# Kernel tuning notes

Measured on AMD Instinct MI355X. Metric: run time of the kernel, lower is better.

Reference implementation:

```python
import jax, jax.numpy as jnp
import numpy as np

NUM_HEADS = 8
MASK_NEG = -1e30


def setup_inputs() -> dict:
    key = jax.random.key(0)
    k1, k2, k3 = jax.random.split(key, 3)
    B, S, D = 8, 2048, 128
    queries = jax.random.normal(k1, (B, S, D), dtype=jnp.float32)
    mask = jnp.ones((B, S), dtype=jnp.float32)
    # kernel_size=1 Conv1D with no bias == dense matmul over last dim
    W_q = jax.random.normal(k2, (D, D), dtype=jnp.float32) * (D ** -0.5)
    W_mem = jax.random.normal(k3, (D, 2 * D), dtype=jnp.float32) * (D ** -0.5)
    return {"queries": queries, "mask": mask, "W_q": W_q, "W_mem": W_mem}


def _split_heads(x, h):
    # [B, S, D] -> [B, h, S, D/h]
    B, S, D = x.shape
    return x.reshape(B, S, h, D // h).transpose(0, 2, 1, 3)


def reference(queries, mask, W_q, W_mem):
    B, S, D = queries.shape
    h = NUM_HEADS
    scale = (D // h) ** -0.5
    memory = jnp.einsum('bsd,de->bse', queries, W_mem)   # [B,S,2D]
    query = jnp.einsum('bsd,de->bse', queries, W_q)      # [B,S,D]
    K, V = jnp.split(memory, 2, axis=2)
    Q = _split_heads(query, h) * scale                   # [B,h,S,dh]
    K = _split_heads(K, h)
    V = _split_heads(V, h)
    logits = jnp.einsum('bhqd,bhkd->bhqk', Q, K)         # [B,h,S,S]
    m = mask.reshape(B, 1, 1, S)
    logits = logits + (1.0 - m) * MASK_NEG
    weights = jax.nn.softmax(logits, axis=-1)
    # dropout is identity at inference (training=None)
    x = jnp.einsum('bhqk,bhkd->bhqd', weights, V)        # [B,h,S,dh]
    return x.transpose(0, 2, 1, 3).reshape(B, S, D)
```

## Files before the change

kernel.cpp:

```cpp
#include <hip/hip_runtime.h>
#include <hip/hip_bf16.h>
#include <stdint.h>

#define B_    8
#define S_    2048
#define D_    128
#define H_    8
#define DH_   16
#define BH_   64
#define E_    384
#define NT_   (S_ / 32)

typedef __attribute__((ext_vector_type(4)))  short short4v;
typedef __attribute__((ext_vector_type(8)))  short short8;
typedef __attribute__((ext_vector_type(4)))  float f32x4;
typedef __attribute__((ext_vector_type(16))) float f32x16;

__device__ inline unsigned short f2b(float f) {
    union { __bf16 h; unsigned short u; } t;
    t.h = (__bf16)f;
    return t.u;
}
__device__ inline float b2f(unsigned short u) {
    union { unsigned u; float f; } x; x.u = ((unsigned)u) << 16; return x.f;
}
__device__ inline int dperm(int d) {
    return (d & 3) | ((d & 8) >> 1) | ((d & 4) << 1);
}

#define EXPB 16250.7346f

__global__ void wtrans_kernel(const float* __restrict__ Wq,
                              const float* __restrict__ Wmem,
                              unsigned short* __restrict__ wt) {
    int e = blockIdx.x, k = threadIdx.x;
    float v = (e < 128) ? Wq[k * 128 + e] : Wmem[k * 256 + (e - 128)];
    wt[e * 128 + k] = f2b(v);
}

__global__ __launch_bounds__(512) void proj_kernel(
        const float* __restrict__ X, const float* __restrict__ mask,
        const unsigned short* __restrict__ wt,
        unsigned short* __restrict__ Qb, unsigned short* __restrict__ Kb,
        unsigned short* __restrict__ Vf) {
    __shared__ unsigned short Xs[64][136];
    __shared__ unsigned short Vs[64][136];
    __shared__ float Ms[64];
    const int tid = threadIdx.x;
    const int b = blockIdx.x & 7, st = blockIdx.x >> 3;
    const int s0 = st * 64;
    const float* Xp = X + ((size_t)b * S_ + s0) * D_;

    for (int i = tid; i < 64 * D_ / 4; i += 512) {
        float4 v = ((const float4*)Xp)[i];
        int row = i >> 5, c4 = (i & 31) * 4;
        Xs[row][c4 + 0] = f2b(v.x); Xs[row][c4 + 1] = f2b(v.y);
        Xs[row][c4 + 2] = f2b(v.z); Xs[row][c4 + 3] = f2b(v.w);
    }
    if (tid < 64) Ms[tid] = mask[(size_t)b * S_ + s0 + tid];
    __syncthreads();

    const int wid = tid >> 6, lane = tid & 63;
    const int lr = lane & 15, lg = lane >> 4;
    const float qscale = 0.25f * 1.44269504088896f;

    for (int ci = 0; ci < 3; ++ci) {
        const int ct = wid + ci * 8;
        const int e0 = ct * 16;
        short4v bfr[8];
        #pragma unroll
        for (int kk = 0; kk < 8; ++kk)
            bfr[kk] = *(const short4v*)&wt[(e0 + lr) * 128 + kk * 16 + lg * 4];
        for (int rt = 0; rt < 4; ++rt) {
            f32x4 acc; acc[0] = acc[1] = acc[2] = acc[3] = 0.f;
            #pragma unroll
            for (int kk = 0; kk < 8; ++kk) {
                short4v a = *(const short4v*)&Xs[rt * 16 + lr][kk * 16 + lg * 4];
                acc = __builtin_amdgcn_mfma_f32_16x16x16bf16_1k(a, bfr[kk], acc, 0, 0, 0);
            }
            const int e = e0 + lr;
            #pragma unroll
            for (int r = 0; r < 4; ++r) {
                const int sl = rt * 16 + lg * 4 + r;
                const float v = acc[r];
                if (e < 128) {
                    int hh = e >> 4, d = dperm(e & 15);
                    Qb[(((size_t)b * H_ + hh) * S_ + s0 + sl) * DH_ + d] = f2b(v * qscale);
                } else if (e < 256) {
                    int ek = e - 128, hh = ek >> 4, d = dperm(ek & 15);
                    Kb[(((size_t)b * H_ + hh) * S_ + s0 + sl) * DH_ + d] = f2b(v);
                } else {
                    Vs[sl][e - 256] = f2b(v);
                }
            }
        }
    }
    __syncthreads();

    for (int j = tid; j < H_ * 2 * 2 * 64; j += 512) {
        const int l = j & 63, f = (j >> 6) & 1, t = (j >> 7) & 1, hh = j >> 8;
        const int q = l & 31, h = l >> 5;
        const int vrow = (q < 16) ? q : 16;
        const int T = st * 2 + t;
        unsigned short* dst =
            Vf + ((((size_t)(b * H_ + hh) * NT_ + T) * 2 + f) * 64 + l) * 8;
        union { unsigned short us[8]; short8 v; } o;
        #pragma unroll
        for (int e = 0; e < 8; ++e) {
            const int p = f * 16 + 8 * h + e;
            const int sl = (p & 16) | dperm(p & 15);
            const int srow = t * 32 + sl;
            const float mk = Ms[srow];
            o.us[e] = f2b((vrow == 16) ? mk : b2f(Vs[srow][hh * 16 + vrow]) * mk);
        }
        *(short8*)dst = o.v;
    }
}

__global__ __launch_bounds__(512, 8) void attn_kernel(
        const unsigned short* __restrict__ Qb, const unsigned short* __restrict__ Kb,
        const unsigned short* __restrict__ Vf, float* __restrict__ out) {
    const int tid = threadIdx.x;
    const int wid = tid >> 6, lane = tid & 63;
    const int q = lane & 31, h = lane >> 5;
    const int p = blockIdx.x;
    const int bh = (p & 7) * 8 + ((p >> 3) & 7);
    const int qt = p >> 6;
    const int q0 = qt * 128 + (wid >> 1) * 32;
    const int ttBase = (wid & 1) * (NT_ / 2);
    const int ttEnd  = ttBase + NT_ / 2;

    const unsigned short* Kp = Kb + (size_t)bh * S_ * DH_ + 8 * h;
    const unsigned short* vfl = Vf + (size_t)bh * NT_ * 1024 + (size_t)lane * 8;

    const short8 qf = *(const short8*)&Qb[((size_t)bh * S_ + q0 + q) * DH_ + 8 * h];

    f32x16 acc, z;
    #pragma unroll
    for (int i = 0; i < 16; ++i) { acc[i] = 0.f; z[i] = 0.f; }

    #pragma unroll 2
    for (int tt = ttBase; tt < ttEnd; ++tt) {
        const short8 kf  = *(const short8*)&Kp[(size_t)(tt * 32 + q) * DH_];
        const short8 va0 = *(const short8*)&vfl[(size_t)tt * 1024];
        const short8 va1 = *(const short8*)&vfl[(size_t)tt * 1024 + 512];

        __builtin_amdgcn_s_setprio(1);
        f32x16 s0 = __builtin_amdgcn_mfma_f32_32x32x16_bf16(kf, qf, z, 0, 0, 0);
        __builtin_amdgcn_s_setprio(0);

        union { unsigned u[4]; short8 v; } b0, b1;
        #pragma unroll
        for (int i = 0; i < 4; ++i) {
            const int l0 = (int)__builtin_fmaf(s0[2 * i],     128.f, EXPB);
            const int h0 = (int)__builtin_fmaf(s0[2 * i + 1], 128.f, EXPB);
            b0.u[i] = (unsigned)l0 | ((unsigned)h0 << 16);
            const int l1 = (int)__builtin_fmaf(s0[8 + 2 * i],     128.f, EXPB);
            const int h1 = (int)__builtin_fmaf(s0[8 + 2 * i + 1], 128.f, EXPB);
            b1.u[i] = (unsigned)l1 | ((unsigned)h1 << 16);
        }
        __builtin_amdgcn_s_setprio(1);
        acc = __builtin_amdgcn_mfma_f32_32x32x16_bf16(va0, b0.v, acc, 0, 0, 0);
        acc = __builtin_amdgcn_mfma_f32_32x32x16_bf16(va1, b1.v, acc, 0, 0, 0);
        __builtin_amdgcn_s_setprio(0);
    }

    __shared__ float cmb[4][16][64];
    if (wid & 1) {
        #pragma unroll
        for (int i = 0; i < 16; ++i)
            cmb[wid >> 1][i][lane] = acc[i];
    }
    __syncthreads();
    if (!(wid & 1)) {
        const int b = bh >> 3, head = bh & 7;
        float* obase = out + ((size_t)b * S_ + q0 + q) * D_ + head * DH_ + 4 * h;
        float o[16];
        #pragma unroll
        for (int i = 0; i < 16; ++i) o[i] = acc[i] + cmb[wid >> 1][i][lane];
        const float r = 1.0f / o[8];
        *(float4*)obase       = make_float4(o[0] * r, o[1] * r, o[2] * r, o[3] * r);
        *(float4*)(obase + 8) = make_float4(o[4] * r, o[5] * r, o[6] * r, o[7] * r);
    }
}

extern "C" void kernel_launch(void* const* d_in, const int* in_sizes, int n_in,
                              void* d_out, int out_size, void* d_ws, size_t ws_size,
                              hipStream_t stream) {
    const float* X    = (const float*)d_in[0];
    const float* mask = (const float*)d_in[1];
    const float* Wq   = (const float*)d_in[2];
    const float* Wmem = (const float*)d_in[3];
    float* out = (float*)d_out;

    unsigned short* Qb = (unsigned short*)d_ws;
    unsigned short* Kb = Qb + (size_t)BH_ * S_ * DH_;
    unsigned short* Vf = Kb + (size_t)BH_ * S_ * DH_;
    unsigned short* wt = Vf + (size_t)BH_ * NT_ * 2 * 64 * 8;

    wtrans_kernel<<<E_, 128, 0, stream>>>(Wq, Wmem, wt);
    proj_kernel<<<B_ * S_ / 64, 512, 0, stream>>>(X, mask, wt, Qb, Kb, Vf);
    attn_kernel<<<BH_ * (S_ / 128), 512, 0, stream>>>(Qb, Kb, Vf, out);
}
```

Measured before the change: 58.57 us.

## Prefetch K/V fragments in attention loop, store K in fragment layout

K is now written by the projection kernel in a per-tile fragment layout (lane-contiguous 8-element chunks), so each lane in the attention kernel does one contiguous 16-byte load per tile instead of a strided gather. The attention loop becomes manually software-pipelined with double-buffered registers, so the next tiles' K/V loads are issued while the current tile computes. Launch bounds drop to 4 waves per SIMD to leave more registers for the prefetch buffers. Nontemporal loads for X and nontemporal stores for the output aim to reduce cache pollution. The cost is higher register pressure and lower occupancy.

```diff
diff --git a/kernel.cpp b/kernel.cpp
--- a/kernel.cpp
+++ b/kernel.cpp
@@ -41,7 +41,7 @@
 __global__ __launch_bounds__(512) void proj_kernel(
         const float* __restrict__ X, const float* __restrict__ mask,
         const unsigned short* __restrict__ wt,
-        unsigned short* __restrict__ Qb, unsigned short* __restrict__ Kb,
+        unsigned short* __restrict__ Qb, unsigned short* __restrict__ Kf,
         unsigned short* __restrict__ Vf) {
     __shared__ unsigned short Xs[64][136];
     __shared__ unsigned short Vs[64][136];
@@ -52,10 +52,10 @@
     const float* Xp = X + ((size_t)b * S_ + s0) * D_;
 
     for (int i = tid; i < 64 * D_ / 4; i += 512) {
-        float4 v = ((const float4*)Xp)[i];
+        f32x4 v = __builtin_nontemporal_load((const f32x4*)Xp + i);
         int row = i >> 5, c4 = (i & 31) * 4;
-        Xs[row][c4 + 0] = f2b(v.x); Xs[row][c4 + 1] = f2b(v.y);
-        Xs[row][c4 + 2] = f2b(v.z); Xs[row][c4 + 3] = f2b(v.w);
+        Xs[row][c4 + 0] = f2b(v[0]); Xs[row][c4 + 1] = f2b(v[1]);
+        Xs[row][c4 + 2] = f2b(v[2]); Xs[row][c4 + 3] = f2b(v[3]);
     }
     if (tid < 64) Ms[tid] = mask[(size_t)b * S_ + s0 + tid];
     __syncthreads();
@@ -88,7 +88,9 @@
                     Qb[(((size_t)b * H_ + hh) * S_ + s0 + sl) * DH_ + d] = f2b(v * qscale);
                 } else if (e < 256) {
                     int ek = e - 128, hh = ek >> 4, d = dperm(ek & 15);
-                    Kb[(((size_t)b * H_ + hh) * S_ + s0 + sl) * DH_ + d] = f2b(v);
+                    int T = st * 2 + (sl >> 5), qq = sl & 31;
+                    int l = qq + 32 * (d >> 3), j = d & 7;
+                    Kf[(((size_t)(b * H_ + hh) * NT_ + T) * 64 + l) * 8 + j] = f2b(v);
                 } else {
                     Vs[sl][e - 256] = f2b(v);
                 }
@@ -117,8 +119,8 @@
     }
 }
 
-__global__ __launch_bounds__(512, 8) void attn_kernel(
-        const unsigned short* __restrict__ Qb, const unsigned short* __restrict__ Kb,
+__global__ __launch_bounds__(512, 4) void attn_kernel(
+        const unsigned short* __restrict__ Qb, const unsigned short* __restrict__ Kf,
         const unsigned short* __restrict__ Vf, float* __restrict__ out) {
     const int tid = threadIdx.x;
     const int wid = tid >> 6, lane = tid & 63;
@@ -130,7 +132,7 @@
     const int ttBase = (wid & 1) * (NT_ / 2);
     const int ttEnd  = ttBase + NT_ / 2;
 
-    const unsigned short* Kp = Kb + (size_t)bh * S_ * DH_ + 8 * h;
+    const unsigned short* kfl = Kf + (size_t)bh * S_ * DH_ + (size_t)lane * 8;
     const unsigned short* vfl = Vf + (size_t)bh * NT_ * 1024 + (size_t)lane * 8;
 
     const short8 qf = *(const short8*)&Qb[((size_t)bh * S_ + q0 + q) * DH_ + 8 * h];
@@ -139,31 +141,48 @@
     #pragma unroll
     for (int i = 0; i < 16; ++i) { acc[i] = 0.f; z[i] = 0.f; }
 
-    #pragma unroll 2
-    for (int tt = ttBase; tt < ttEnd; ++tt) {
-        const short8 kf  = *(const short8*)&Kp[(size_t)(tt * 32 + q) * DH_];
-        const short8 va0 = *(const short8*)&vfl[(size_t)tt * 1024];
-        const short8 va1 = *(const short8*)&vfl[(size_t)tt * 1024 + 512];
-
-        __builtin_amdgcn_s_setprio(1);
-        f32x16 s0 = __builtin_amdgcn_mfma_f32_32x32x16_bf16(kf, qf, z, 0, 0, 0);
-        __builtin_amdgcn_s_setprio(0);
-
-        union { unsigned u[4]; short8 v; } b0, b1;
-        #pragma unroll
-        for (int i = 0; i < 4; ++i) {
-            const int l0 = (int)__builtin_fmaf(s0[2 * i],     128.f, EXPB);
-            const int h0 = (int)__builtin_fmaf(s0[2 * i + 1], 128.f, EXPB);
-            b0.u[i] = (unsigned)l0 | ((unsigned)h0 << 16);
-            const int l1 = (int)__builtin_fmaf(s0[8 + 2 * i],     128.f, EXPB);
-            const int h1 = (int)__builtin_fmaf(s0[8 + 2 * i + 1], 128.f, EXPB);
-            b1.u[i] = (unsigned)l1 | ((unsigned)h1 << 16);
-        }
-        __builtin_amdgcn_s_setprio(1);
-        acc = __builtin_amdgcn_mfma_f32_32x32x16_bf16(va0, b0.v, acc, 0, 0, 0);
-        acc = __builtin_amdgcn_mfma_f32_32x32x16_bf16(va1, b1.v, acc, 0, 0, 0);
-        __builtin_amdgcn_s_setprio(0);
-    }
+    short8 kb0, kb1, v0b0, v0b1, v1b0, v1b1;
+    kb0  = *(const short8*)&kfl[(size_t)ttBase * 512];
+    v0b0 = *(const short8*)&vfl[(size_t)ttBase * 1024];
+    v1b0 = *(const short8*)&vfl[(size_t)ttBase * 1024 + 512];
+    kb1  = *(const short8*)&kfl[(size_t)(ttBase + 1) * 512];
+    v0b1 = *(const short8*)&vfl[(size_t)(ttBase + 1) * 1024];
+    v1b1 = *(const short8*)&vfl[(size_t)(ttBase + 1) * 1024 + 512];
+
+#define ATTN_TILE(KF_, V0_, V1_)                                               \
+    {                                                                          \
+        __builtin_amdgcn_s_setprio(1);                                         \
+        f32x16 s0 = __builtin_amdgcn_mfma_f32_32x32x16_bf16(KF_, qf, z, 0, 0, 0); \
+        __builtin_amdgcn_s_setprio(0);                                         \
+        union { unsigned u[4]; short8 v; } b0, b1;                             \
+        _Pragma("unroll")                                                      \
+        for (int i = 0; i < 4; ++i) {                                          \
+            const int l0 = (int)__builtin_fmaf(s0[2 * i],     128.f, EXPB);    \
+            const int h0 = (int)__builtin_fmaf(s0[2 * i + 1], 128.f, EXPB);    \
+            b0.u[i] = (unsigned)l0 | ((unsigned)h0 << 16);                     \
+            const int l1 = (int)__builtin_fmaf(s0[8 + 2 * i],     128.f, EXPB);\
+            const int h1 = (int)__builtin_fmaf(s0[8 + 2 * i + 1], 128.f, EXPB);\
+            b1.u[i] = (unsigned)l1 | ((unsigned)h1 << 16);                     \
+        }                                                                      \
+        __builtin_amdgcn_s_setprio(1);                                         \
+        acc = __builtin_amdgcn_mfma_f32_32x32x16_bf16(V0_, b0.v, acc, 0, 0, 0);\
+        acc = __builtin_amdgcn_mfma_f32_32x32x16_bf16(V1_, b1.v, acc, 0, 0, 0);\
+        __builtin_amdgcn_s_setprio(0);                                         \
+    }
+
+    for (int tt = ttBase; tt < ttEnd - 2; tt += 2) {
+        ATTN_TILE(kb0, v0b0, v1b0);
+        kb0  = *(const short8*)&kfl[(size_t)(tt + 2) * 512];
+        v0b0 = *(const short8*)&vfl[(size_t)(tt + 2) * 1024];
+        v1b0 = *(const short8*)&vfl[(size_t)(tt + 2) * 1024 + 512];
+        ATTN_TILE(kb1, v0b1, v1b1);
+        kb1  = *(const short8*)&kfl[(size_t)(tt + 3) * 512];
+        v0b1 = *(const short8*)&vfl[(size_t)(tt + 3) * 1024];
+        v1b1 = *(const short8*)&vfl[(size_t)(tt + 3) * 1024 + 512];
+    }
+    ATTN_TILE(kb0, v0b0, v1b0);
+    ATTN_TILE(kb1, v0b1, v1b1);
+#undef ATTN_TILE
 
     __shared__ float cmb[4][16][64];
     if (wid & 1) {
@@ -179,8 +198,11 @@
         #pragma unroll
         for (int i = 0; i < 16; ++i) o[i] = acc[i] + cmb[wid >> 1][i][lane];
         const float r = 1.0f / o[8];
-        *(float4*)obase       = make_float4(o[0] * r, o[1] * r, o[2] * r, o[3] * r);
-        *(float4*)(obase + 8) = make_float4(o[4] * r, o[5] * r, o[6] * r, o[7] * r);
+        f32x4 o0, o1;
+        o0[0] = o[0] * r; o0[1] = o[1] * r; o0[2] = o[2] * r; o0[3] = o[3] * r;
+        o1[0] = o[4] * r; o1[1] = o[5] * r; o1[2] = o[6] * r; o1[3] = o[7] * r;
+        __builtin_nontemporal_store(o0, (f32x4*)obase);
+        __builtin_nontemporal_store(o1, (f32x4*)(obase + 8));
     }
 }
 
@@ -194,11 +216,11 @@
     float* out = (float*)d_out;
 
     unsigned short* Qb = (unsigned short*)d_ws;
-    unsigned short* Kb = Qb + (size_t)BH_ * S_ * DH_;
-    unsigned short* Vf = Kb + (size_t)BH_ * S_ * DH_;
+    unsigned short* Kf = Qb + (size_t)BH_ * S_ * DH_;
+    unsigned short* Vf = Kf + (size_t)BH_ * S_ * DH_;
     unsigned short* wt = Vf + (size_t)BH_ * NT_ * 2 * 64 * 8;
 
     wtrans_kernel<<<E_, 128, 0, stream>>>(Wq, Wmem, wt);
-    proj_kernel<<<B_ * S_ / 64, 512, 0, stream>>>(X, mask, wt, Qb, Kb, Vf);
-    attn_kernel<<<BH_ * (S_ / 128), 512, 0, stream>>>(Qb, Kb, Vf, out);
-}
+    proj_kernel<<<B_ * S_ / 64, 512, 0, stream>>>(X, mask, wt, Qb, Kf, Vf);
+    attn_kernel<<<BH_ * (S_ / 128), 512, 0, stream>>>(Qb, Kf, Vf, out);
+}
```

Result: no change. 59.48 us (+1.6%).

## Stage K/V tiles through LDS with async global_load_lds ring buffer in attention

Applied to the files above, without the earlier changes.

The attention kernel now shares K and V tile loads across the block. Six waves issue direct global-to-LDS loads into a 4-deep ring buffer, and every wave reads its fragments from LDS, replacing per-wave redundant global loads. K is re-laid out in the projection kernel into a fragment-ordered format so each staging load is one contiguous 16-byte-per-lane copy. The X load becomes a nontemporal load and the occupancy hint drops to 4 blocks per CU. The cost is two block barriers per iteration, which can stall the MFMA/exp pipeline, and the lower occupancy hint may reduce latency hiding.

```diff
diff --git a/kernel.cpp b/kernel.cpp
--- a/kernel.cpp
+++ b/kernel.cpp
@@ -28,6 +28,12 @@
     return (d & 3) | ((d & 8) >> 1) | ((d & 4) << 1);
 }
 
+__device__ inline void gload_lds16(const void* g, void* l) {
+    __builtin_amdgcn_global_load_lds(
+        (const __attribute__((address_space(1))) unsigned int*)g,
+        (__attribute__((address_space(3))) unsigned int*)l, 16, 0, 0);
+}
+
 #define EXPB 16250.7346f
 
 __global__ void wtrans_kernel(const float* __restrict__ Wq,
@@ -41,7 +47,7 @@
 __global__ __launch_bounds__(512) void proj_kernel(
         const float* __restrict__ X, const float* __restrict__ mask,
         const unsigned short* __restrict__ wt,
-        unsigned short* __restrict__ Qb, unsigned short* __restrict__ Kb,
+        unsigned short* __restrict__ Qb, unsigned short* __restrict__ Kf,
         unsigned short* __restrict__ Vf) {
     __shared__ unsigned short Xs[64][136];
     __shared__ unsigned short Vs[64][136];
@@ -52,10 +58,10 @@
     const float* Xp = X + ((size_t)b * S_ + s0) * D_;
 
     for (int i = tid; i < 64 * D_ / 4; i += 512) {
-        float4 v = ((const float4*)Xp)[i];
+        f32x4 v = __builtin_nontemporal_load((const f32x4*)Xp + i);
         int row = i >> 5, c4 = (i & 31) * 4;
-        Xs[row][c4 + 0] = f2b(v.x); Xs[row][c4 + 1] = f2b(v.y);
-        Xs[row][c4 + 2] = f2b(v.z); Xs[row][c4 + 3] = f2b(v.w);
+        Xs[row][c4 + 0] = f2b(v[0]); Xs[row][c4 + 1] = f2b(v[1]);
+        Xs[row][c4 + 2] = f2b(v[2]); Xs[row][c4 + 3] = f2b(v[3]);
     }
     if (tid < 64) Ms[tid] = mask[(size_t)b * S_ + s0 + tid];
     __syncthreads();
@@ -88,7 +94,9 @@
                     Qb[(((size_t)b * H_ + hh) * S_ + s0 + sl) * DH_ + d] = f2b(v * qscale);
                 } else if (e < 256) {
                     int ek = e - 128, hh = ek >> 4, d = dperm(ek & 15);
-                    Kb[(((size_t)b * H_ + hh) * S_ + s0 + sl) * DH_ + d] = f2b(v);
+                    int T = st * 2 + (sl >> 5), qq = sl & 31;
+                    int l = qq + 32 * (d >> 3), j = d & 7;
+                    Kf[(((size_t)(b * H_ + hh) * NT_ + T) * 64 + l) * 8 + j] = f2b(v);
                 } else {
                     Vs[sl][e - 256] = f2b(v);
                 }
@@ -117,8 +125,8 @@
     }
 }
 
-__global__ __launch_bounds__(512, 8) void attn_kernel(
-        const unsigned short* __restrict__ Qb, const unsigned short* __restrict__ Kb,
+__global__ __launch_bounds__(512, 4) void attn_kernel(
+        const unsigned short* __restrict__ Qb, const unsigned short* __restrict__ Kf,
         const unsigned short* __restrict__ Vf, float* __restrict__ out) {
     const int tid = threadIdx.x;
     const int wid = tid >> 6, lane = tid & 63;
@@ -127,11 +135,12 @@
     const int bh = (p & 7) * 8 + ((p >> 3) & 7);
     const int qt = p >> 6;
     const int q0 = qt * 128 + (wid >> 1) * 32;
-    const int ttBase = (wid & 1) * (NT_ / 2);
-    const int ttEnd  = ttBase + NT_ / 2;
-
-    const unsigned short* Kp = Kb + (size_t)bh * S_ * DH_ + 8 * h;
-    const unsigned short* vfl = Vf + (size_t)bh * NT_ * 1024 + (size_t)lane * 8;
+    const int hf = wid & 1;
+
+    __shared__ unsigned short ldsKV[4][6][64][8];
+
+    const unsigned short* ksrc = Kf + (size_t)bh * S_ * DH_;
+    const unsigned short* vsrc = Vf + (size_t)bh * NT_ * 1024;
 
     const short8 qf = *(const short8*)&Qb[((size_t)bh * S_ + q0 + q) * DH_ + 8 * h];
 
@@ -139,11 +148,35 @@
     #pragma unroll
     for (int i = 0; i < 16; ++i) { acc[i] = 0.f; z[i] = 0.f; }
 
-    #pragma unroll 2
-    for (int tt = ttBase; tt < ttEnd; ++tt) {
-        const short8 kf  = *(const short8*)&Kp[(size_t)(tt * 32 + q) * DH_];
-        const short8 va0 = *(const short8*)&vfl[(size_t)tt * 1024];
-        const short8 va1 = *(const short8*)&vfl[(size_t)tt * 1024 + 512];
+    const int s_h3 = wid / 3, s_s = wid % 3;
+
+#define STAGE(JS_)                                                             \
+    if (wid < 6) {                                                             \
+        const int js_ = (JS_);                                                 \
+        const int tt_ = s_h3 * 32 + js_;                                       \
+        const unsigned short* gp_ =                                            \
+            (s_s == 0) ? ksrc + (size_t)tt_ * 512 + lane * 8                   \
+                       : vsrc + (size_t)tt_ * 1024 + (s_s - 1) * 512 + lane * 8;\
+        gload_lds16(gp_, &ldsKV[js_ & 3][wid][0][0]);                          \
+    }
+
+    STAGE(0); STAGE(1); STAGE(2); STAGE(3);
+
+    for (int j = 0; j < 32; ++j) {
+        asm volatile("s_waitcnt vmcnt(3)" ::: "memory");
+        __builtin_amdgcn_s_barrier();
+        asm volatile("" ::: "memory");
+
+        const int slot = j & 3;
+        const short8 kf  = *(const short8*)&ldsKV[slot][3 * hf + 0][lane][0];
+        const short8 va0 = *(const short8*)&ldsKV[slot][3 * hf + 1][lane][0];
+        const short8 va1 = *(const short8*)&ldsKV[slot][3 * hf + 2][lane][0];
+
+        asm volatile("s_waitcnt lgkmcnt(0)" ::: "memory");
+        __builtin_amdgcn_s_barrier();
+        asm volatile("" ::: "memory");
+
+        STAGE((j + 4) & 31);
 
         __builtin_amdgcn_s_setprio(1);
         f32x16 s0 = __builtin_amdgcn_mfma_f32_32x32x16_bf16(kf, qf, z, 0, 0, 0);
@@ -164,8 +197,12 @@
         acc = __builtin_amdgcn_mfma_f32_32x32x16_bf16(va1, b1.v, acc, 0, 0, 0);
         __builtin_amdgcn_s_setprio(0);
     }
-
-    __shared__ float cmb[4][16][64];
+#undef STAGE
+
+    asm volatile("s_waitcnt vmcnt(0)" ::: "memory");
+    __syncthreads();
+
+    float (*cmb)[16][64] = (float (*)[16][64]) & ldsKV[0][0][0][0];
     if (wid & 1) {
         #pragma unroll
         for (int i = 0; i < 16; ++i)
@@ -194,11 +231,11 @@
     float* out = (float*)d_out;
 
     unsigned short* Qb = (unsigned short*)d_ws;
-    unsigned short* Kb = Qb + (size_t)BH_ * S_ * DH_;
-    unsigned short* Vf = Kb + (size_t)BH_ * S_ * DH_;
+    unsigned short* Kf = Qb + (size_t)BH_ * S_ * DH_;
+    unsigned short* Vf = Kf + (size_t)BH_ * S_ * DH_;
     unsigned short* wt = Vf + (size_t)BH_ * NT_ * 2 * 64 * 8;
 
     wtrans_kernel<<<E_, 128, 0, stream>>>(Wq, Wmem, wt);
-    proj_kernel<<<B_ * S_ / 64, 512, 0, stream>>>(X, mask, wt, Qb, Kb, Vf);
-    attn_kernel<<<BH_ * (S_ / 128), 512, 0, stream>>>(Qb, Kb, Vf, out);
-}
+    proj_kernel<<<B_ * S_ / 64, 512, 0, stream>>>(X, mask, wt, Qb, Kf, Vf);
+    attn_kernel<<<BH_ * (S_ / 128), 512, 0, stream>>>(Qb, Kf, Vf, out);
+}
```

Result: slower. 62.31 us (+6.4%).
